# Performance work log

Hardware: AMD Instinct MI355X
Metric: run time of the kernel (lower is better)

The kernel has to match this reference:

```python
import jax, jax.numpy as jnp
import numpy as np

EPS = 1e-5

def _layernorm(x, g, b):
    mu = jnp.mean(x, axis=-1, keepdims=True)
    var = jnp.var(x, axis=-1, keepdims=True)
    return (x - mu) * jax.lax.rsqrt(var + EPS) * g + b

def _pos_encoding(S, D, dtype):
    pos = jnp.arange(S, dtype=jnp.float32)[:, None]
    div = jnp.exp(jnp.arange(0, D, 2, dtype=jnp.float32) * (-jnp.log(10000.0) / D))
    pe = jnp.zeros((S, D), dtype=jnp.float32)
    pe = pe.at[:, 0::2].set(jnp.sin(pos * div))
    pe = pe.at[:, 1::2].set(jnp.cos(pos * div))
    return pe.astype(dtype)

def setup_inputs() -> dict:
    key = jax.random.key(0)
    B, S, D, H, F, L = 4, 1024, 768, 12, 3072, 6
    ks = jax.random.split(key, 8)
    s = 0.02
    return {
        "x": jax.random.normal(ks[0], (B, S, D), jnp.float32),
        "Wqkv": jax.random.normal(ks[1], (L, D, 3 * D), jnp.float32) * s,
        "bqkv": jnp.zeros((L, 3 * D), jnp.float32),
        "Wo": jax.random.normal(ks[2], (L, D, D), jnp.float32) * s,
        "bo": jnp.zeros((L, D), jnp.float32),
        "ln1_g": jnp.ones((L, D), jnp.float32),
        "ln1_b": jnp.zeros((L, D), jnp.float32),
        "W1": jax.random.normal(ks[3], (L, D, F), jnp.float32) * s,
        "b1": jnp.zeros((L, F), jnp.float32),
        "W2": jax.random.normal(ks[4], (L, F, D), jnp.float32) * s,
        "b2": jnp.zeros((L, D), jnp.float32),
        "ln2_g": jnp.ones((L, D), jnp.float32),
        "ln2_b": jnp.zeros((L, D), jnp.float32),
        "lnf_g": jnp.ones((D,), jnp.float32),
        "lnf_b": jnp.zeros((D,), jnp.float32),
        "num_heads": 12,
    }

def reference(x, Wqkv, bqkv, Wo, bo, ln1_g, ln1_b, W1, b1, W2, b2, ln2_g, ln2_b, lnf_g, lnf_b, num_heads):
    B, S, D = x.shape
    H = num_heads
    hd = D // H
    scale = 1.0 / jnp.sqrt(jnp.float32(hd)).astype(x.dtype)

    x = x + _pos_encoding(S, D, x.dtype)[None]

    def layer(h, params):
        wqkv, bq, wo, bo_, g1, b1_, w1, bias1, w2, bias2, g2, b2_ = params
        qkv = (h @ wqkv + bq).reshape(B, S, 3, H, hd)
        q, k, v = jnp.moveaxis(qkv, 2, 0)          # each [B,S,H,hd]
        q = q.transpose(0, 2, 1, 3)                 # bhqd
        k = k.transpose(0, 2, 1, 3)
        v = v.transpose(0, 2, 1, 3)
        scores = jnp.einsum('bhqd,bhkd->bhqk', q, k) * scale
        w = jax.nn.softmax(scores, axis=-1)
        w = jnp.clip(w, 1e-6, 1.0)                  # clamp as in torch module
        attn = jnp.einsum('bhqk,bhkd->bhqd', w, v)
        attn = attn.transpose(0, 2, 1, 3).reshape(B, S, D) @ wo + bo_
        h = _layernorm(h + attn, g1, b1_)
        ffn = jax.nn.relu(h @ w1 + bias1) @ w2 + bias2
        h = _layernorm(h + ffn, g2, b2_)
        return h, None

    params = (Wqkv, bqkv, Wo, bo, ln1_g, ln1_b, W1, b1, W2, b2, ln2_g, ln2_b)
    x, _ = jax.lax.scan(layer, x, params)
    return _layernorm(x, lnf_g, lnf_b)
```

## Files before the change

kernel.cpp:

```cpp
#include <hip/hip_runtime.h>
#include <math.h>

typedef float f32x4 __attribute__((ext_vector_type(4)));
typedef __bf16 bf16x8 __attribute__((ext_vector_type(8)));
typedef unsigned short u16x8 __attribute__((ext_vector_type(8)));

__device__ __forceinline__ unsigned short f2bf(float f) {
    union { float f; unsigned int u; } v; v.f = f;
    unsigned int r = v.u + 0x7FFFu + ((v.u >> 16) & 1u);
    return (unsigned short)(r >> 16);
}
__device__ __forceinline__ unsigned short f2bft(float f) {
    union { float f; unsigned int u; } v; v.f = f;
    return (unsigned short)(v.u >> 16);
}
__device__ __forceinline__ float bf2f(unsigned short u) {
    union { unsigned int u; float f; } v; v.u = ((unsigned int)u) << 16;
    return v.f;
}
__device__ __forceinline__ bf16x8 ld8(const unsigned short* p) {
    union { u16x8 u; bf16x8 b; } c;
    c.u = *(const u16x8*)p;
    return c.b;
}
__device__ __forceinline__ void gload_lds16(const unsigned short* g, unsigned short* l) {
    __builtin_amdgcn_global_load_lds(
        (const __attribute__((address_space(1))) unsigned int*)g,
        (__attribute__((address_space(3))) unsigned int*)l,
        16, 0, 0);
}
__device__ __forceinline__ int swz_off(int row, int quad) {
    return row * 32 + ((quad ^ ((row >> 1) & 3)) << 3);
}

__global__ __launch_bounds__(256)
void wprep_k(const float* __restrict__ Wqkv, const float* __restrict__ Wo,
             const float* __restrict__ W1, const float* __restrict__ W2,
             unsigned short* __restrict__ qkvT, unsigned short* __restrict__ woT,
             unsigned short* __restrict__ w1T, unsigned short* __restrict__ w2T) {
    __shared__ float tile[32][33];
    int bid = blockIdx.x;
    const float* W; unsigned short* Wt; int K, N, idx;
    if (bid < 1728)      { W = Wqkv; Wt = qkvT; K = 768;  N = 2304; idx = bid; }
    else if (bid < 2304) { W = Wo;   Wt = woT;  K = 768;  N = 768;  idx = bid - 1728; }
    else if (bid < 4608) { W = W1;   Wt = w1T;  K = 768;  N = 3072; idx = bid - 2304; }
    else                 { W = W2;   Wt = w2T;  K = 3072; N = 768;  idx = bid - 4608; }
    int ntile = N / 32;
    int n0 = (idx % ntile) * 32, k0 = (idx / ntile) * 32;
    int tx = threadIdx.x & 31, ty = threadIdx.x >> 5;
#pragma unroll
    for (int i = 0; i < 4; ++i) {
        int k = ty + i * 8;
        tile[k][tx] = W[(size_t)(k0 + k) * N + n0 + tx];
    }
    __syncthreads();
#pragma unroll
    for (int i = 0; i < 4; ++i) {
        int n = ty + i * 8;
        Wt[(size_t)(n0 + n) * K + k0 + tx] = f2bf(tile[tx][n]);
    }
}

__global__ __launch_bounds__(256)
void posenc_k(const float* __restrict__ x, float* __restrict__ h,
              unsigned short* __restrict__ hb) {
    int idx = blockIdx.x * 256 + threadIdx.x;
    const int TOT = 4 * 1024 * 768;
    if (idx >= TOT) return;
    int d = idx % 768;
    int s = (idx / 768) % 1024;
    int i2 = d >> 1;
    float dv = expf(-(float)(2 * i2) * (9.210340371976184f / 768.0f));
    float ang = (float)s * dv;
    float pe = (d & 1) ? cosf(ang) : sinf(ang);
    float v = x[idx] + pe;
    h[idx] = v;
    hb[idx] = f2bf(v);
}

template<int RELU, int BIAS>
__global__ __launch_bounds__(256)
void gemm_k(const unsigned short* __restrict__ A, const unsigned short* __restrict__ Bt,
            const float* __restrict__ bias, unsigned short* __restrict__ Cb,
            int M, int N, int K, int Kc) {
    __shared__ unsigned short As[2][128 * 32];
    __shared__ unsigned short Bs[2][128 * 32];
    const int tid = threadIdx.x;
    const int lane = tid & 63, wave = tid >> 6;
    const int l15 = lane & 15, quad = lane >> 4;
    const int m0 = blockIdx.y * 128, n0 = blockIdx.x * 128;
    const int wr = (wave >> 1) * 64, wc = (wave & 1) * 64;
    const int kstart = blockIdx.z * Kc;
    unsigned short* Cbp = Cb + (size_t)blockIdx.z * M * N;

    const int r0 = wave * 32 + (lane >> 2);
    const int kc0 = lane & 3;

    auto stage = [&](int k0, int bi) {
#pragma unroll
        for (int j = 0; j < 2; ++j) {
            int r = r0 + j * 16;
            int kcl = kc0 ^ ((r >> 1) & 3);
            gload_lds16(A + (size_t)(m0 + r) * K + k0 + kcl * 8,
                        &As[bi][(wave * 32 + j * 16) * 32]);
            gload_lds16(Bt + (size_t)(n0 + r) * K + k0 + kcl * 8,
                        &Bs[bi][(wave * 32 + j * 16) * 32]);
        }
    };

    f32x4 acc[4][4];
#pragma unroll
    for (int i = 0; i < 4; ++i)
#pragma unroll
        for (int j = 0; j < 4; ++j) acc[i][j] = (f32x4){0.f, 0.f, 0.f, 0.f};

    stage(kstart, 0);
    const int nk = Kc / 32;
    for (int t = 0; t < nk; ++t) {
        __syncthreads();
        if (t + 1 < nk) stage(kstart + (t + 1) * 32, (t + 1) & 1);
        const unsigned short* Asb = As[t & 1];
        const unsigned short* Bsb = Bs[t & 1];
        bf16x8 af[4], bfr[4];
#pragma unroll
        for (int mt = 0; mt < 4; ++mt)
            af[mt] = ld8(&Asb[swz_off(wr + mt * 16 + l15, quad)]);
#pragma unroll
        for (int nt = 0; nt < 4; ++nt)
            bfr[nt] = ld8(&Bsb[swz_off(wc + nt * 16 + l15, quad)]);
#pragma unroll
        for (int mt = 0; mt < 4; ++mt)
#pragma unroll
            for (int nt = 0; nt < 4; ++nt)
                acc[mt][nt] = __builtin_amdgcn_mfma_f32_16x16x32_bf16(
                    af[mt], bfr[nt], acc[mt][nt], 0, 0, 0);
    }
#pragma unroll
    for (int mt = 0; mt < 4; ++mt)
#pragma unroll
        for (int nt = 0; nt < 4; ++nt)
#pragma unroll
            for (int r = 0; r < 4; ++r) {
                int row = m0 + wr + mt * 16 + quad * 4 + r;
                int col = n0 + wc + nt * 16 + l15;
                float v = acc[mt][nt][r];
                if (BIAS) v += bias[col];
                if (RELU) v = fmaxf(v, 0.f);
                Cbp[(size_t)row * N + col] = f2bf(v);
            }
}

__global__ __launch_bounds__(256)
void qkv_prep(const unsigned short* __restrict__ qkv, unsigned short* __restrict__ Q,
              unsigned short* __restrict__ Ko, unsigned short* __restrict__ Vt) {
    __shared__ unsigned short t[64][65];
    int bh = blockIdx.y, s0 = blockIdx.x * 64;
    int b = bh / 12, h = bh % 12;
    int tid = threadIdx.x;
    int tx = tid & 63, ty = tid >> 6;
#pragma unroll
    for (int r = 0; r < 16; ++r) {
        int i = ty + r * 4;
        t[i][tx] = qkv[(size_t)(b * 1024 + s0 + i) * 2304 + 1536 + h * 64 + tx];
    }
    const float QS = 0.18033688088889765f;
#pragma unroll
    for (int it = 0; it < 2; ++it) {
        int task = tid + it * 256;
        int row = task >> 3, ch = (task & 7) * 8;
        size_t src = (size_t)(b * 1024 + s0 + row) * 2304 + h * 64 + ch;
        u16x8 qv = *(const u16x8*)&qkv[src];
#pragma unroll
        for (int j = 0; j < 8; ++j) qv[j] = f2bf(bf2f(qv[j]) * QS);
        *(u16x8*)&Q[((size_t)bh * 1024 + s0 + row) * 64 + ch] = qv;
        u16x8 kv = *(const u16x8*)&qkv[src + 768];
        *(u16x8*)&Ko[((size_t)bh * 1024 + s0 + row) * 64 + ch] = kv;
    }
    __syncthreads();
#pragma unroll
    for (int r = 0; r < 16; ++r) {
        int dd = ty + r * 4;
        Vt[((size_t)bh * 64 + dd) * 1024 + s0 + tx] = t[tx][dd];
    }
}

__global__ __launch_bounds__(256)
void flash_k(const unsigned short* __restrict__ Q, const unsigned short* __restrict__ K,
             const unsigned short* __restrict__ Vt, unsigned short* __restrict__ O2,
             float* __restrict__ ls) {
    const int S = 1024, HD = 64;
    int bh = blockIdx.y, b = bh / 12, h = bh % 12;
    int q0 = blockIdx.x * 64;
    int zz = blockIdx.z;
    const unsigned short* Qp = Q + ((size_t)bh * S + q0) * HD;
    const unsigned short* Kp = K + (size_t)bh * S * HD;
    const unsigned short* Vp = Vt + (size_t)bh * HD * S;

    __shared__ unsigned short sm[12288];
    unsigned short* Qs = sm;
    unsigned short* Ks = sm + 4096;
    unsigned short* Vs = sm + 8192;

    int tid = threadIdx.x, lane = tid & 63, wave = tid >> 6;
    int l15 = lane & 15, quad = lane >> 4;
    const int rl0 = lane >> 2, c0 = lane & 3;

#pragma unroll
    for (int j = 0; j < 2; ++j) {
        int R = wave * 32 + j * 16 + rl0;
        int khalf = R >> 6, grow = R & 63;
        int lch = c0 ^ ((R >> 1) & 3);
        gload_lds16(Qp + grow * HD + khalf * 32 + lch * 8,
                    &Qs[(wave * 32 + j * 16) * 32]);
    }
    __syncthreads();
    bf16x8 qa0 = ld8(&Qs[swz_off(wave * 16 + l15, quad)]);
    bf16x8 qa1 = ld8(&Qs[swz_off(64 + wave * 16 + l15, quad)]);

    f32x4 o[4];
#pragma unroll
    for (int i = 0; i < 4; ++i) o[i] = (f32x4){0.f, 0.f, 0.f, 0.f};
    f32x4 lacc = (f32x4){0.f, 0.f, 0.f, 0.f};
    bf16x8 ones;
    {
        union { u16x8 u; bf16x8 b; } c;
#pragma unroll
        for (int j = 0; j < 8; ++j) c.u[j] = 0x3F80;
        ones = c.b;
    }
    unsigned short* Pw = sm + wave * 1024;

    for (int kt = zz * 8; kt < zz * 8 + 8; ++kt) {
        __syncthreads();
#pragma unroll
        for (int j = 0; j < 2; ++j) {
            int R = wave * 32 + j * 16 + rl0;
            int khalf = R >> 6, grow = R & 63;
            int lch = c0 ^ ((R >> 1) & 3);
            gload_lds16(Kp + (kt * 64 + grow) * HD + khalf * 32 + lch * 8,
                        &Ks[(wave * 32 + j * 16) * 32]);
            gload_lds16(Vp + (size_t)grow * S + kt * 64 + khalf * 32 + lch * 8,
                        &Vs[(wave * 32 + j * 16) * 32]);
        }
        __syncthreads();

        f32x4 sc[4];
#pragma unroll
        for (int cb = 0; cb < 4; ++cb) {
            bf16x8 kb0 = ld8(&Ks[swz_off(cb * 16 + l15, quad)]);
            bf16x8 kb1 = ld8(&Ks[swz_off(64 + cb * 16 + l15, quad)]);
            f32x4 z = (f32x4){0.f, 0.f, 0.f, 0.f};
            z = __builtin_amdgcn_mfma_f32_16x16x32_bf16(qa0, kb0, z, 0, 0, 0);
            z = __builtin_amdgcn_mfma_f32_16x16x32_bf16(qa1, kb1, z, 0, 0, 0);
            sc[cb] = z;
        }
#pragma unroll
        for (int cb = 0; cb < 4; ++cb)
#pragma unroll
            for (int r = 0; r < 4; ++r)
                Pw[(quad * 4 + r) * 64 + ((cb * 16 + l15) ^ (quad << 4))] =
                    f2bft(__builtin_amdgcn_exp2f(sc[cb][r]));
        bf16x8 pa0 = ld8(&Pw[l15 * 64 + ((quad * 8) ^ ((l15 >> 2) << 4))]);
        bf16x8 pa1 = ld8(&Pw[l15 * 64 + ((32 + quad * 8) ^ ((l15 >> 2) << 4))]);
        lacc = __builtin_amdgcn_mfma_f32_16x16x32_bf16(pa0, ones, lacc, 0, 0, 0);
        lacc = __builtin_amdgcn_mfma_f32_16x16x32_bf16(pa1, ones, lacc, 0, 0, 0);
#pragma unroll
        for (int cb = 0; cb < 4; ++cb) {
            bf16x8 vb0 = ld8(&Vs[swz_off(cb * 16 + l15, quad)]);
            bf16x8 vb1 = ld8(&Vs[swz_off(64 + cb * 16 + l15, quad)]);
            o[cb] = __builtin_amdgcn_mfma_f32_16x16x32_bf16(pa0, vb0, o[cb], 0, 0, 0);
            o[cb] = __builtin_amdgcn_mfma_f32_16x16x32_bf16(pa1, vb1, o[cb], 0, 0, 0);
        }
    }
    unsigned short* Op = O2 + (size_t)zz * 4096 * 768;
#pragma unroll
    for (int cb = 0; cb < 4; ++cb)
#pragma unroll
        for (int r = 0; r < 4; ++r) {
            int row = q0 + wave * 16 + quad * 4 + r;
            Op[((size_t)(b * 1024 + row)) * 768 + h * 64 + cb * 16 + l15] =
                f2bf(o[cb][r]);
        }
    if (l15 == 0) {
#pragma unroll
        for (int r = 0; r < 4; ++r)
            ls[zz * 49152 + bh * 1024 + q0 + wave * 16 + quad * 4 + r] = lacc[r];
    }
}

__global__ __launch_bounds__(256)
void attn_combine_k(const unsigned short* __restrict__ O2, const float* __restrict__ ls,
                    unsigned short* __restrict__ ctx) {
    int idx = blockIdx.x * 256 + threadIdx.x;
    int ch = idx % 96;
    int row = idx / 96;
    int col = ch * 8;
    int b = row >> 10, s = row & 1023, h = col >> 6;
    const size_t MD = (size_t)4096 * 768;
    u16x8 o0 = *(const u16x8*)&O2[(size_t)row * 768 + col];
    u16x8 o1 = *(const u16x8*)&O2[MD + (size_t)row * 768 + col];
    int li = (b * 12 + h) * 1024 + s;
    float rl = 1.0f / (ls[li] + ls[49152 + li]);
    u16x8 ov;
#pragma unroll
    for (int j = 0; j < 8; ++j)
        ov[j] = f2bf((bf2f(o0[j]) + bf2f(o1[j])) * rl);
    *(u16x8*)&ctx[(size_t)row * 768 + col] = ov;
}

template<int NPART, int WBF16>
__global__ __launch_bounds__(256)
void ln_k(const float* __restrict__ X, const unsigned short* __restrict__ P,
          const float* __restrict__ pb,
          const float* __restrict__ g, const float* __restrict__ bta,
          float* __restrict__ Yf, unsigned short* __restrict__ Yb) {
    const int D = 768;
    const size_t MD = (size_t)4096 * 768;
    int row = blockIdx.x;
    int tid = threadIdx.x;
    const float* x = X + (size_t)row * D;
    float v[3];
    float s = 0.f, s2 = 0.f;
#pragma unroll
    for (int i = 0; i < 3; ++i) {
        int c = i * 256 + tid;
        float t = x[c];
        if (NPART > 0) {
            float r = pb[c];
#pragma unroll
            for (int pi = 0; pi < NPART; ++pi)
                r += bf2f(P[MD * pi + (size_t)row * D + c]);
            t += r;
        }
        v[i] = t;
        s += t;
        s2 += t * t;
    }
#pragma unroll
    for (int off = 1; off < 64; off <<= 1) {
        s += __shfl_xor(s, off);
        s2 += __shfl_xor(s2, off);
    }
    __shared__ float rs[4], rs2[4];
    int wave = tid >> 6, lane = tid & 63;
    if (lane == 0) { rs[wave] = s; rs2[wave] = s2; }
    __syncthreads();
    s = rs[0] + rs[1] + rs[2] + rs[3];
    s2 = rs2[0] + rs2[1] + rs2[2] + rs2[3];
    float mu = s * (1.f / 768.f);
    float var = s2 * (1.f / 768.f) - mu * mu;
    float rstd = rsqrtf(var + 1e-5f);
#pragma unroll
    for (int i = 0; i < 3; ++i) {
        int c = i * 256 + tid;
        float y = (v[i] - mu) * rstd * g[c] + bta[c];
        Yf[(size_t)row * D + c] = y;
        if (WBF16) Yb[(size_t)row * D + c] = f2bf(y);
    }
}

extern "C" void kernel_launch(void* const* d_in, const int* in_sizes, int n_in,
                              void* d_out, int out_size, void* d_ws, size_t ws_size,
                              hipStream_t stream) {
    const float* x    = (const float*)d_in[0];
    const float* Wqkv = (const float*)d_in[1];
    const float* bqkv = (const float*)d_in[2];
    const float* Wo   = (const float*)d_in[3];
    const float* bo   = (const float*)d_in[4];
    const float* ln1g = (const float*)d_in[5];
    const float* ln1b = (const float*)d_in[6];
    const float* W1   = (const float*)d_in[7];
    const float* b1   = (const float*)d_in[8];
    const float* W2   = (const float*)d_in[9];
    const float* b2   = (const float*)d_in[10];
    const float* ln2g = (const float*)d_in[11];
    const float* ln2b = (const float*)d_in[12];
    const float* lnfg = (const float*)d_in[13];
    const float* lnfb = (const float*)d_in[14];

    const int B = 4, S = 1024, D = 768, H = 12, F = 3072, L = 6;
    const int M = B * S;

    char* p = (char*)d_ws;
    auto alloc = [&](size_t bytes) -> char* {
        char* r = p;
        p += (bytes + 255) & ~(size_t)255;
        return r;
    };
    float* h             = (float*)alloc((size_t)M * D * 4);
    unsigned short* tmp  = (unsigned short*)alloc((size_t)4 * M * D * 2);
    float* lsbuf         = (float*)alloc((size_t)2 * 48 * 1024 * 4);
    unsigned short* hb   = (unsigned short*)alloc((size_t)M * D * 2);
    unsigned short* act  = (unsigned short*)alloc((size_t)M * F * 2);
    unsigned short* Qb   = (unsigned short*)alloc((size_t)M * D * 2);
    unsigned short* Kb   = (unsigned short*)alloc((size_t)M * D * 2);
    unsigned short* Vtb  = (unsigned short*)alloc((size_t)M * D * 2);
    unsigned short* ctx  = (unsigned short*)alloc((size_t)M * D * 2);
    unsigned short* wqkvT = (unsigned short*)alloc((size_t)3 * D * D * 2);
    unsigned short* woT   = (unsigned short*)alloc((size_t)D * D * 2);
    unsigned short* w1T   = (unsigned short*)alloc((size_t)D * F * 2);
    unsigned short* w2T   = (unsigned short*)alloc((size_t)D * F * 2);
    unsigned short* qkvb = act;
    unsigned short* f1b  = act;

    posenc_k<<<(M * D) / 256, 256, 0, stream>>>(x, h, hb);

    for (int l = 0; l < L; ++l) {
        wprep_k<<<6912, 256, 0, stream>>>(
            Wqkv + (size_t)l * D * 3 * D, Wo + (size_t)l * D * D,
            W1 + (size_t)l * D * F, W2 + (size_t)l * F * D,
            wqkvT, woT, w1T, w2T);

        gemm_k<0, 1><<<dim3(3 * D / 128, M / 128, 1), 256, 0, stream>>>(
            hb, wqkvT, bqkv + (size_t)l * 3 * D, qkvb, M, 3 * D, D, D);
        qkv_prep<<<dim3(S / 64, B * H), 256, 0, stream>>>(qkvb, Qb, Kb, Vtb);
        flash_k<<<dim3(S / 64, B * H, 2), 256, 0, stream>>>(Qb, Kb, Vtb, tmp, lsbuf);
        attn_combine_k<<<(M * 96) / 256, 256, 0, stream>>>(tmp, lsbuf, ctx);
        gemm_k<0, 0><<<dim3(D / 128, M / 128, 4), 256, 0, stream>>>(
            ctx, woT, nullptr, tmp, M, D, D, D / 4);
        ln_k<4, 1><<<M, 256, 0, stream>>>(h, tmp, bo + (size_t)l * D,
                                          ln1g + (size_t)l * D, ln1b + (size_t)l * D,
                                          h, hb);
        gemm_k<1, 1><<<dim3(F / 128, M / 128, 1), 256, 0, stream>>>(
            hb, w1T, b1 + (size_t)l * F, f1b, M, F, D, D);
        gemm_k<0, 0><<<dim3(D / 128, M / 128, 4), 256, 0, stream>>>(
            f1b, w2T, nullptr, tmp, M, D, F, F / 4);
        ln_k<4, 1><<<M, 256, 0, stream>>>(h, tmp, b2 + (size_t)l * D,
                                          ln2g + (size_t)l * D, ln2b + (size_t)l * D,
                                          h, hb);
    }
    ln_k<0, 0><<<M, 256, 0, stream>>>(h, nullptr, nullptr, lnfg, lnfb,
                                      (float*)d_out, nullptr);
}
```

Baseline: 1.226 ms.

## Fold Q scaling into QKV GEMM, read Q/K in place, batch weight prep

Applies the softmax scale to the Q columns inside the QKV GEMM epilogue and has the flash kernel read Q and K directly from the strided QKV buffer. This removes the Q/K copy kernel work, and the prep kernel now only transposes V. It also converts all six layers' weights to bf16 in a single launch when the workspace is large enough, replacing six per-layer launches. The strided Q/K loads may coalesce less well, and the batched weight prep needs a larger workspace.

```diff
diff --git a/kernel.cpp b/kernel.cpp
--- a/kernel.cpp
+++ b/kernel.cpp
@@ -40,11 +40,12 @@
              unsigned short* __restrict__ w1T, unsigned short* __restrict__ w2T) {
     __shared__ float tile[32][33];
     int bid = blockIdx.x;
+    size_t ly = blockIdx.y;
     const float* W; unsigned short* Wt; int K, N, idx;
-    if (bid < 1728)      { W = Wqkv; Wt = qkvT; K = 768;  N = 2304; idx = bid; }
-    else if (bid < 2304) { W = Wo;   Wt = woT;  K = 768;  N = 768;  idx = bid - 1728; }
-    else if (bid < 4608) { W = W1;   Wt = w1T;  K = 768;  N = 3072; idx = bid - 2304; }
-    else                 { W = W2;   Wt = w2T;  K = 3072; N = 768;  idx = bid - 4608; }
+    if (bid < 1728)      { W = Wqkv + ly * 768 * 2304; Wt = qkvT + ly * 768 * 2304; K = 768;  N = 2304; idx = bid; }
+    else if (bid < 2304) { W = Wo   + ly * 768 * 768;  Wt = woT  + ly * 768 * 768;  K = 768;  N = 768;  idx = bid - 1728; }
+    else if (bid < 4608) { W = W1   + ly * 768 * 3072; Wt = w1T  + ly * 768 * 3072; K = 768;  N = 3072; idx = bid - 2304; }
+    else                 { W = W2   + ly * 3072 * 768; Wt = w2T  + ly * 3072 * 768; K = 3072; N = 768;  idx = bid - 4608; }
     int ntile = N / 32;
     int n0 = (idx % ntile) * 32, k0 = (idx / ntile) * 32;
     int tx = threadIdx.x & 31, ty = threadIdx.x >> 5;
@@ -78,7 +79,7 @@
     hb[idx] = f2bf(v);
 }
 
-template<int RELU, int BIAS>
+template<int RELU, int BIAS, int QSCALE>
 __global__ __launch_bounds__(256)
 void gemm_k(const unsigned short* __restrict__ A, const unsigned short* __restrict__ Bt,
             const float* __restrict__ bias, unsigned short* __restrict__ Cb,
@@ -135,6 +136,7 @@
                 acc[mt][nt] = __builtin_amdgcn_mfma_f32_16x16x32_bf16(
                     af[mt], bfr[nt], acc[mt][nt], 0, 0, 0);
     }
+    const float scl = (QSCALE && n0 < 768) ? 0.18033688088889765f : 1.0f;
 #pragma unroll
     for (int mt = 0; mt < 4; ++mt)
 #pragma unroll
@@ -145,14 +147,14 @@
                 int col = n0 + wc + nt * 16 + l15;
                 float v = acc[mt][nt][r];
                 if (BIAS) v += bias[col];
+                if (QSCALE) v *= scl;
                 if (RELU) v = fmaxf(v, 0.f);
                 Cbp[(size_t)row * N + col] = f2bf(v);
             }
 }
 
 __global__ __launch_bounds__(256)
-void qkv_prep(const unsigned short* __restrict__ qkv, unsigned short* __restrict__ Q,
-              unsigned short* __restrict__ Ko, unsigned short* __restrict__ Vt) {
+void vt_prep(const unsigned short* __restrict__ qkv, unsigned short* __restrict__ Vt) {
     __shared__ unsigned short t[64][65];
     int bh = blockIdx.y, s0 = blockIdx.x * 64;
     int b = bh / 12, h = bh % 12;
@@ -163,19 +165,6 @@
         int i = ty + r * 4;
         t[i][tx] = qkv[(size_t)(b * 1024 + s0 + i) * 2304 + 1536 + h * 64 + tx];
     }
-    const float QS = 0.18033688088889765f;
-#pragma unroll
-    for (int it = 0; it < 2; ++it) {
-        int task = tid + it * 256;
-        int row = task >> 3, ch = (task & 7) * 8;
-        size_t src = (size_t)(b * 1024 + s0 + row) * 2304 + h * 64 + ch;
-        u16x8 qv = *(const u16x8*)&qkv[src];
-#pragma unroll
-        for (int j = 0; j < 8; ++j) qv[j] = f2bf(bf2f(qv[j]) * QS);
-        *(u16x8*)&Q[((size_t)bh * 1024 + s0 + row) * 64 + ch] = qv;
-        u16x8 kv = *(const u16x8*)&qkv[src + 768];
-        *(u16x8*)&Ko[((size_t)bh * 1024 + s0 + row) * 64 + ch] = kv;
-    }
     __syncthreads();
 #pragma unroll
     for (int r = 0; r < 16; ++r) {
@@ -185,15 +174,14 @@
 }
 
 __global__ __launch_bounds__(256)
-void flash_k(const unsigned short* __restrict__ Q, const unsigned short* __restrict__ K,
-             const unsigned short* __restrict__ Vt, unsigned short* __restrict__ O2,
-             float* __restrict__ ls) {
+void flash_k(const unsigned short* __restrict__ QKV, const unsigned short* __restrict__ Vt,
+             unsigned short* __restrict__ O2, float* __restrict__ ls) {
     const int S = 1024, HD = 64;
     int bh = blockIdx.y, b = bh / 12, h = bh % 12;
     int q0 = blockIdx.x * 64;
     int zz = blockIdx.z;
-    const unsigned short* Qp = Q + ((size_t)bh * S + q0) * HD;
-    const unsigned short* Kp = K + (size_t)bh * S * HD;
+    const unsigned short* Qp = QKV + (size_t)(b * 1024 + q0) * 2304 + h * 64;
+    const unsigned short* Kp = QKV + (size_t)(b * 1024) * 2304 + 768 + h * 64;
     const unsigned short* Vp = Vt + (size_t)bh * HD * S;
 
     __shared__ unsigned short sm[12288];
@@ -210,7 +198,7 @@
         int R = wave * 32 + j * 16 + rl0;
         int khalf = R >> 6, grow = R & 63;
         int lch = c0 ^ ((R >> 1) & 3);
-        gload_lds16(Qp + grow * HD + khalf * 32 + lch * 8,
+        gload_lds16(Qp + (size_t)grow * 2304 + khalf * 32 + lch * 8,
                     &Qs[(wave * 32 + j * 16) * 32]);
     }
     __syncthreads();
@@ -237,7 +225,7 @@
             int R = wave * 32 + j * 16 + rl0;
             int khalf = R >> 6, grow = R & 63;
             int lch = c0 ^ ((R >> 1) & 3);
-            gload_lds16(Kp + (kt * 64 + grow) * HD + khalf * 32 + lch * 8,
+            gload_lds16(Kp + (size_t)(kt * 64 + grow) * 2304 + khalf * 32 + lch * 8,
                         &Ks[(wave * 32 + j * 16) * 32]);
             gload_lds16(Vp + (size_t)grow * S + kt * 64 + khalf * 32 + lch * 8,
                         &Vs[(wave * 32 + j * 16) * 32]);
@@ -381,6 +369,8 @@
     const int B = 4, S = 1024, D = 768, H = 12, F = 3072, L = 6;
     const int M = B * S;
 
+    const int WL = (ws_size >= (size_t)200 * 1024 * 1024) ? 6 : 1;
+
     char* p = (char*)d_ws;
     auto alloc = [&](size_t bytes) -> char* {
         char* r = p;
@@ -392,39 +382,46 @@
     float* lsbuf         = (float*)alloc((size_t)2 * 48 * 1024 * 4);
     unsigned short* hb   = (unsigned short*)alloc((size_t)M * D * 2);
     unsigned short* act  = (unsigned short*)alloc((size_t)M * F * 2);
-    unsigned short* Qb   = (unsigned short*)alloc((size_t)M * D * 2);
-    unsigned short* Kb   = (unsigned short*)alloc((size_t)M * D * 2);
     unsigned short* Vtb  = (unsigned short*)alloc((size_t)M * D * 2);
     unsigned short* ctx  = (unsigned short*)alloc((size_t)M * D * 2);
-    unsigned short* wqkvT = (unsigned short*)alloc((size_t)3 * D * D * 2);
-    unsigned short* woT   = (unsigned short*)alloc((size_t)D * D * 2);
-    unsigned short* w1T   = (unsigned short*)alloc((size_t)D * F * 2);
-    unsigned short* w2T   = (unsigned short*)alloc((size_t)D * F * 2);
+    unsigned short* wqkvT = (unsigned short*)alloc((size_t)WL * 3 * D * D * 2);
+    unsigned short* woT   = (unsigned short*)alloc((size_t)WL * D * D * 2);
+    unsigned short* w1T   = (unsigned short*)alloc((size_t)WL * D * F * 2);
+    unsigned short* w2T   = (unsigned short*)alloc((size_t)WL * D * F * 2);
     unsigned short* qkvb = act;
     unsigned short* f1b  = act;
 
     posenc_k<<<(M * D) / 256, 256, 0, stream>>>(x, h, hb);
+    if (WL == 6)
+        wprep_k<<<dim3(6912, 6), 256, 0, stream>>>(Wqkv, Wo, W1, W2,
+                                                   wqkvT, woT, w1T, w2T);
 
     for (int l = 0; l < L; ++l) {
-        wprep_k<<<6912, 256, 0, stream>>>(
-            Wqkv + (size_t)l * D * 3 * D, Wo + (size_t)l * D * D,
-            W1 + (size_t)l * D * F, W2 + (size_t)l * F * D,
-            wqkvT, woT, w1T, w2T);
-
-        gemm_k<0, 1><<<dim3(3 * D / 128, M / 128, 1), 256, 0, stream>>>(
-            hb, wqkvT, bqkv + (size_t)l * 3 * D, qkvb, M, 3 * D, D, D);
-        qkv_prep<<<dim3(S / 64, B * H), 256, 0, stream>>>(qkvb, Qb, Kb, Vtb);
-        flash_k<<<dim3(S / 64, B * H, 2), 256, 0, stream>>>(Qb, Kb, Vtb, tmp, lsbuf);
+        if (WL == 1)
+            wprep_k<<<dim3(6912, 1), 256, 0, stream>>>(
+                Wqkv + (size_t)l * D * 3 * D, Wo + (size_t)l * D * D,
+                W1 + (size_t)l * D * F, W2 + (size_t)l * F * D,
+                wqkvT, woT, w1T, w2T);
+        size_t lo = (WL == 6) ? (size_t)l : 0;
+        const unsigned short* qT  = wqkvT + lo * 3 * D * D;
+        const unsigned short* oT  = woT   + lo * D * D;
+        const unsigned short* f1T = w1T   + lo * D * F;
+        const unsigned short* f2T = w2T   + lo * D * F;
+
+        gemm_k<0, 1, 1><<<dim3(3 * D / 128, M / 128, 1), 256, 0, stream>>>(
+            hb, qT, bqkv + (size_t)l * 3 * D, qkvb, M, 3 * D, D, D);
+        vt_prep<<<dim3(S / 64, B * H), 256, 0, stream>>>(qkvb, Vtb);
+        flash_k<<<dim3(S / 64, B * H, 2), 256, 0, stream>>>(qkvb, Vtb, tmp, lsbuf);
         attn_combine_k<<<(M * 96) / 256, 256, 0, stream>>>(tmp, lsbuf, ctx);
-        gemm_k<0, 0><<<dim3(D / 128, M / 128, 4), 256, 0, stream>>>(
-            ctx, woT, nullptr, tmp, M, D, D, D / 4);
+        gemm_k<0, 0, 0><<<dim3(D / 128, M / 128, 4), 256, 0, stream>>>(
+            ctx, oT, nullptr, tmp, M, D, D, D / 4);
         ln_k<4, 1><<<M, 256, 0, stream>>>(h, tmp, bo + (size_t)l * D,
                                           ln1g + (size_t)l * D, ln1b + (size_t)l * D,
                                           h, hb);
-        gemm_k<1, 1><<<dim3(F / 128, M / 128, 1), 256, 0, stream>>>(
-            hb, w1T, b1 + (size_t)l * F, f1b, M, F, D, D);
-        gemm_k<0, 0><<<dim3(D / 128, M / 128, 4), 256, 0, stream>>>(
-            f1b, w2T, nullptr, tmp, M, D, F, F / 4);
+        gemm_k<1, 1, 0><<<dim3(F / 128, M / 128, 1), 256, 0, stream>>>(
+            hb, f1T, b1 + (size_t)l * F, f1b, M, F, D, D);
+        gemm_k<0, 0, 0><<<dim3(D / 128, M / 128, 4), 256, 0, stream>>>(
+            f1b, f2T, nullptr, tmp, M, D, F, F / 4);
         ln_k<4, 1><<<M, 256, 0, stream>>>(h, tmp, b2 + (size_t)l * D,
                                           ln2g + (size_t)l * D, ln2b + (size_t)l * D,
                                           h, hb);
```

Result: faster. 1.193 ms (-2.7%).
